# Optimization experiments

Hardware: AMD Instinct MI355X
Metric: run time of the kernel (lower is better)

The kernel has to match this reference:

```python
import jax, jax.numpy as jnp
import numpy as np

D_MODEL = 1024
NUM_HEADS = 16
SEQ = 2048
BATCH = 4
THETA = 10000.0
D_K = D_MODEL // NUM_HEADS


def setup_inputs() -> dict:
    key = jax.random.key(0)
    k1, k2, k3, k4, k5 = jax.random.split(key, 5)
    std = np.sqrt(2.0 / (D_MODEL + D_MODEL))
    x = jax.random.normal(k1, (BATCH, SEQ, D_MODEL), dtype=jnp.float32)
    wq = jax.random.normal(k2, (D_MODEL, D_MODEL), dtype=jnp.float32) * std
    wk = jax.random.normal(k3, (D_MODEL, D_MODEL), dtype=jnp.float32) * std
    wv = jax.random.normal(k4, (D_MODEL, D_MODEL), dtype=jnp.float32) * std
    wo = jax.random.normal(k5, (D_MODEL, D_MODEL), dtype=jnp.float32) * std
    token_positions = jnp.arange(SEQ, dtype=jnp.int32)
    return {"x": x, "wq": wq, "wk": wk, "wv": wv, "wo": wo,
            "token_positions": token_positions}


def _apply_rope(t, cos, sin):
    # t: (b, h, s, d_k); cos/sin: (s, d_k/2) -> broadcast over (b, h)
    pairs = t.reshape(*t.shape[:-1], D_K // 2, 2)
    x0, x1 = pairs[..., 0], pairs[..., 1]
    r0 = x0 * cos - x1 * sin
    r1 = x0 * sin + x1 * cos
    return jnp.stack((r0, r1), axis=-1).reshape(t.shape)


def reference(x, wq, wk, wv, wo, token_positions):
    b, s, d = x.shape
    h, dk = NUM_HEADS, D_K

    def split_heads(y):  # (b, s, d) -> (b, h, s, d_k)
        return y.reshape(b, s, h, dk).transpose(0, 2, 1, 3)

    q = split_heads(x @ wq.T)
    k = split_heads(x @ wk.T)
    v = split_heads(x @ wv.T)

    # RoPE tables: angles_j = theta^{-(2j)/d_k}, j = 0..d_k/2-1
    inv_freq = 1.0 / (THETA ** (jnp.arange(0, dk, 2, dtype=jnp.float32) / dk))
    ang = token_positions.astype(jnp.float32)[:, None] * inv_freq[None, :]  # (s, d_k/2)
    cos, sin = jnp.cos(ang), jnp.sin(ang)
    q = _apply_rope(q, cos, sin)
    k = _apply_rope(k, cos, sin)

    scores = jnp.einsum('bhqd,bhkd->bhqk', q, k) / jnp.sqrt(jnp.float32(dk))
    causal = jnp.tril(jnp.ones((s, s), dtype=bool))
    scores = jnp.where(causal, scores, -jnp.inf)
    attn = jax.nn.softmax(scores, axis=-1)
    out = jnp.einsum('bhqk,bhkd->bhqd', attn, v)  # (b, h, s, d_k)
    out = out.transpose(0, 2, 1, 3).reshape(b, s, d)
    return out @ wo.T
```

## Files before the change

### kernel.cpp

```cpp
#include <hip/hip_runtime.h>
#include <stdint.h>

#define B_   4
#define S_   2048
#define H_   16
#define DK_  64
#define DM_  1024
#define M_   (B_ * S_)

typedef __attribute__((ext_vector_type(4)))  float f32x4;
typedef __attribute__((ext_vector_type(16))) float f32x16;
typedef __attribute__((ext_vector_type(8)))  short s16x8;

__device__ __forceinline__ uint16_t f2bf(float f) {
    union { float f; uint32_t u; } v; v.f = f;
    uint32_t u = v.u;
    uint32_t r = (u + 0x7FFFu + ((u >> 16) & 1u)) >> 16;
    return (uint16_t)r;
}
__device__ __forceinline__ float bf2f(uint16_t h) {
    union { uint32_t u; float f; } v; v.u = ((uint32_t)h) << 16;
    return v.f;
}
__device__ __forceinline__ uint32_t cvt_pk_bf16(float lo, float hi) {
    uint32_t r;
    asm("v_cvt_pk_bf16_f32 %0, %1, %2" : "=v"(r) : "v"(lo), "v"(hi));
    return r;
}

__device__ __forceinline__ void gload_lds16(const uint16_t* g, uint16_t* l) {
    __builtin_amdgcn_global_load_lds(
        (const __attribute__((address_space(1))) void*)g,
        (__attribute__((address_space(3))) void*)l, 16, 0, 0);
}

__global__ __launch_bounds__(256) void cvt_bf16(const float* __restrict__ in,
                                                uint16_t* __restrict__ out, int n) {
    int i = (blockIdx.x * 256 + threadIdx.x) * 4;
    if (i >= n) return;
    float4 v = *reinterpret_cast<const float4*>(in + i);
    ushort4 o;
    o.x = f2bf(v.x); o.y = f2bf(v.y); o.z = f2bf(v.z); o.w = f2bf(v.w);
    *reinterpret_cast<ushort4*>(out + i) = o;
}

template <int MODE>
__global__ __launch_bounds__(256) void gemm_bt(const uint16_t* __restrict__ A,
                                               const uint16_t* __restrict__ Bm,
                                               void* __restrict__ Cout,
                                               int M, int N, int K) {
    __shared__ uint16_t Al[128 * 32];
    __shared__ uint16_t Bl[128 * 32];
    const int lane = threadIdx.x & 63;
    const int w    = threadIdx.x >> 6;
    const int wr   = w >> 1, wc = w & 1;
    const int m0   = blockIdx.x * 128;
    const int n0   = blockIdx.y * 128;
    const int lr   = lane & 15;
    const int lg   = lane >> 4;

    const int srow = w * 32 + (lane >> 2);
    const int scol = (lane & 3) * 8;
    const uint16_t* Ag = A  + (size_t)(m0 + srow) * K + scol;
    const uint16_t* Bg = Bm + (size_t)(n0 + srow) * K + scol;
    uint16_t* Ald = Al + (size_t)(w * 32) * 32;
    uint16_t* Bld = Bl + (size_t)(w * 32) * 32;

    f32x4 acc[4][4] = {};
    for (int k0 = 0; k0 < K; k0 += 32) {
        gload_lds16(Ag + k0,                  Ald);
        gload_lds16(Ag + 16 * (size_t)K + k0, Ald + 16 * 32);
        gload_lds16(Bg + k0,                  Bld);
        gload_lds16(Bg + 16 * (size_t)K + k0, Bld + 16 * 32);
        __syncthreads();
        s16x8 af[4], bfr[4];
#pragma unroll
        for (int i = 0; i < 4; ++i)
            af[i] = *reinterpret_cast<const s16x8*>(&Al[(wr * 64 + i * 16 + lr) * 32 + lg * 8]);
#pragma unroll
        for (int j = 0; j < 4; ++j)
            bfr[j] = *reinterpret_cast<const s16x8*>(&Bl[(wc * 64 + j * 16 + lr) * 32 + lg * 8]);
#pragma unroll
        for (int i = 0; i < 4; ++i)
#pragma unroll
            for (int j = 0; j < 4; ++j)
                acc[i][j] = __builtin_amdgcn_mfma_f32_16x16x32_bf16(af[i], bfr[j],
                                                                    acc[i][j], 0, 0, 0);
        __syncthreads();
    }

#pragma unroll
    for (int i = 0; i < 4; ++i)
#pragma unroll
        for (int j = 0; j < 4; ++j)
#pragma unroll
            for (int r = 0; r < 4; ++r) {
                int row = wr * 64 + m0 + i * 16 + lg * 4 + r;
                int col = wc * 64 + n0 + j * 16 + lr;
                float v = acc[i][j][r];
                if constexpr (MODE == 0) {
                    ((float*)Cout)[(size_t)row * N + col] = v;
                } else if constexpr (MODE == 1) {
                    int b = row >> 11, s = row & (S_ - 1);
                    int h = col >> 6,  dk = col & 63;
                    ((uint16_t*)Cout)[(((size_t)(b * H_ + h)) * S_ + s) * DK_ + dk] = f2bf(v);
                } else {
                    int h = row >> 6,  dk = row & 63;
                    int b = col >> 11, s = col & (S_ - 1);
                    ((uint16_t*)Cout)[(((size_t)(b * H_ + h)) * DK_ + dk) * S_ + s] = f2bf(v);
                }
            }
}

__global__ __launch_bounds__(256) void gemm_qk(const uint16_t* __restrict__ A,
                                               const uint16_t* __restrict__ wq,
                                               const uint16_t* __restrict__ wk,
                                               uint16_t* __restrict__ qout,
                                               uint16_t* __restrict__ kout) {
    __shared__ uint16_t Al[128 * 32];
    __shared__ uint16_t Bl[128 * 32];
    const int K = DM_;
    const int lane = threadIdx.x & 63;
    const int w    = threadIdx.x >> 6;
    const int wr   = w >> 1, wc = w & 1;
    const int m0   = blockIdx.x * 128;
    const int sel  = blockIdx.y >> 3;
    const int n0   = (blockIdx.y & 7) * 128;
    const uint16_t* Bw = sel ? wk : wq;
    uint16_t* dst      = sel ? kout : qout;
    const int lr   = lane & 15;
    const int lg   = lane >> 4;

    const int srow = w * 32 + (lane >> 2);
    const int scol = (lane & 3) * 8;
    const uint16_t* Ag = A  + (size_t)(m0 + srow) * K + scol;
    const uint16_t* Bg = Bw + (size_t)(n0 + srow) * K + scol;
    uint16_t* Ald = Al + (size_t)(w * 32) * 32;
    uint16_t* Bld = Bl + (size_t)(w * 32) * 32;

    f32x4 acc[4][4] = {};
    for (int k0 = 0; k0 < K; k0 += 32) {
        gload_lds16(Ag + k0,                  Ald);
        gload_lds16(Ag + 16 * (size_t)K + k0, Ald + 16 * 32);
        gload_lds16(Bg + k0,                  Bld);
        gload_lds16(Bg + 16 * (size_t)K + k0, Bld + 16 * 32);
        __syncthreads();
        s16x8 af[4], bfr[4];
#pragma unroll
        for (int i = 0; i < 4; ++i)
            af[i] = *reinterpret_cast<const s16x8*>(&Al[(wr * 64 + i * 16 + lr) * 32 + lg * 8]);
#pragma unroll
        for (int j = 0; j < 4; ++j)
            bfr[j] = *reinterpret_cast<const s16x8*>(&Bl[(wc * 64 + j * 16 + lr) * 32 + lg * 8]);
#pragma unroll
        for (int i = 0; i < 4; ++i)
#pragma unroll
            for (int j = 0; j < 4; ++j)
                acc[i][j] = __builtin_amdgcn_mfma_f32_16x16x32_bf16(af[i], bfr[j],
                                                                    acc[i][j], 0, 0, 0);
        __syncthreads();
    }

#pragma unroll
    for (int i = 0; i < 4; ++i)
#pragma unroll
        for (int j = 0; j < 4; ++j)
#pragma unroll
            for (int r = 0; r < 4; ++r) {
                int row = wr * 64 + m0 + i * 16 + lg * 4 + r;
                int col = wc * 64 + n0 + j * 16 + lr;
                int b = row >> 11, s = row & (S_ - 1);
                int h = col >> 6,  dk = col & 63;
                dst[(((size_t)(b * H_ + h)) * S_ + s) * DK_ + dk] = f2bf(acc[i][j][r]);
            }
}

__global__ __launch_bounds__(256) void rope_kernel(uint16_t* __restrict__ a,
                                                   const int* __restrict__ pos,
                                                   int npairs) {
    int t = blockIdx.x * 256 + threadIdx.x;
    if (t >= npairs) return;
    int j = t & 31;
    int s = (t >> 5) & (S_ - 1);
    float p   = (float)pos[s];
    float inv = exp2f(-(float)j * (13.287712379549449f / 32.0f));
    float ang = p * inv;
    float sn, c;
    sincosf(ang, &sn, &c);
    uint32_t pr = *reinterpret_cast<uint32_t*>(a + (size_t)2 * t);
    float x0 = bf2f((uint16_t)(pr & 0xFFFF));
    float x1 = bf2f((uint16_t)(pr >> 16));
    float r0 = x0 * c - x1 * sn;
    float r1 = x0 * sn + x1 * c;
    uint32_t ot = (uint32_t)f2bf(r0) | ((uint32_t)f2bf(r1) << 16);
    *reinterpret_cast<uint32_t*>(a + (size_t)2 * t) = ot;
}

__global__ __launch_bounds__(256, 2) void flash_attn(const uint16_t* __restrict__ qg,
                                                     const uint16_t* __restrict__ kg,
                                                     const uint16_t* __restrict__ vtg,
                                                     uint16_t* __restrict__ attn) {
    __shared__ __align__(16) uint16_t Kl[2][4096];
    __shared__ __align__(16) uint16_t Vl[2][4096];
    __shared__ __align__(16) uint16_t obuf[4][2048];
    const int lane = threadIdx.x & 63;
    const int w    = threadIdx.x >> 6;
    const int ql   = lane & 31;
    const int hi   = lane >> 5;
    const int id   = blockIdx.x;
    const int bh   = (id & 7) * 8 + ((id >> 3) & 7);
    const int s    = 15 - (id >> 6);
    const int b    = bh >> 4, hh = bh & 15;

    const uint16_t* kb_ = kg  + (size_t)bh * S_ * DK_;
    const uint16_t* vb_ = vtg + (size_t)bh * DK_ * S_;
    const float SC = 0.18033688011112042f;

    char* obb = (char*)&obuf[w][0];
    const int swz = (ql & 7) << 4;

    const int q0 = s * 128 + w * 32;
    const int rowg  = q0 + ql;
    const int ntmax = 2 * s + 2;

    const int srow = lane >> 3;
    const int scol = ((lane & 7) ^ srow) << 3;

    const uint16_t* qp = qg + ((size_t)bh * S_ + q0 + ql) * DK_ + hi * 8;
    s16x8 qf[4];
#pragma unroll
    for (int kk = 0; kk < 4; ++kk)
        qf[kk] = *reinterpret_cast<const s16x8*>(qp + kk * 16);

    f32x16 o0 = {}, o1 = {};
    float l_l = 0.f;

#pragma unroll
    for (int i = 0; i < 2; ++i) {
        gload_lds16(kb_ + (size_t)(w * 16 + i * 8 + srow) * DK_ + scol, &Kl[0][w * 1024 + i * 512]);
        gload_lds16(vb_ + (size_t)(w * 16 + i * 8 + srow) * S_  + scol, &Vl[0][w * 1024 + i * 512]);
    }

    for (int t = 0; t < ntmax; ++t) {
        const int kt  = t * 64;
        const int cur = t & 1;
        __syncthreads();
        if (t + 1 < ntmax) {
            const int kt2 = kt + 64, nb = cur ^ 1;
#pragma unroll
            for (int i = 0; i < 2; ++i) {
                gload_lds16(kb_ + (size_t)(kt2 + w * 16 + i * 8 + srow) * DK_ + scol,
                            &Kl[nb][w * 1024 + i * 512]);
                gload_lds16(vb_ + (size_t)(w * 16 + i * 8 + srow) * S_ + kt2 + scol,
                            &Vl[nb][w * 1024 + i * 512]);
            }
        }
        if (kt > q0 + 31) continue;

        s16x8 kf[8];
#pragma unroll
        for (int kb2 = 0; kb2 < 2; ++kb2)
#pragma unroll
            for (int kk = 0; kk < 4; ++kk)
                kf[kb2 * 4 + kk] = *reinterpret_cast<const s16x8*>(
                    &Kl[cur][(kb2 * 32 + ql) * 64 + (((kk * 32 + hi * 16) ^ swz) >> 1)]);

        f32x16 sc0 = {}, sc1 = {};
        __builtin_amdgcn_s_setprio(1);
#pragma unroll
        for (int kk = 0; kk < 4; ++kk)
            sc0 = __builtin_amdgcn_mfma_f32_32x32x16_bf16(kf[kk], qf[kk], sc0, 0, 0, 0);
#pragma unroll
        for (int kk = 0; kk < 4; ++kk)
            sc1 = __builtin_amdgcn_mfma_f32_32x32x16_bf16(kf[4 + kk], qf[kk], sc1, 0, 0, 0);
        __builtin_amdgcn_s_setprio(0);

        if (kt + 63 > q0) {
            const int keybase = kt + 4 * hi;
#pragma unroll
            for (int r = 0; r < 16; ++r) {
                const int cr = (r & 3) + 8 * (r >> 2);
                if (keybase + cr > rowg)      sc0[r] = -3e38f;
                if (keybase + cr + 32 > rowg) sc1[r] = -3e38f;
            }
        }

#pragma unroll
        for (int r = 0; r < 16; ++r) {
            float p0 = exp2f(sc0[r] * SC);
            float p1 = exp2f(sc1[r] * SC);
            sc0[r] = p0; sc1[r] = p1;
            l_l += p0 + p1;
        }

        s16x8 pf[4];
        {
            union PW { uint32_t u[4]; s16x8 v; };
#pragma unroll
            for (int half = 0; half < 2; ++half) {
                const f32x16& e = half ? sc1 : sc0;
#pragma unroll
                for (int sl = 0; sl < 2; ++sl) {
                    const int rb = sl * 8;
                    uint32_t a0 = cvt_pk_bf16(e[rb + 0], e[rb + 1]);
                    uint32_t b0 = cvt_pk_bf16(e[rb + 4], e[rb + 5]);
                    uint32_t a1 = cvt_pk_bf16(e[rb + 2], e[rb + 3]);
                    uint32_t b1 = cvt_pk_bf16(e[rb + 6], e[rb + 7]);
                    asm("v_permlane32_swap_b32 %0, %1" : "+v"(a0), "+v"(b0));
                    asm("v_permlane32_swap_b32 %0, %1" : "+v"(a1), "+v"(b1));
                    PW pw; pw.u[0] = a0; pw.u[1] = a1; pw.u[2] = b0; pw.u[3] = b1;
                    pf[half * 2 + sl] = pw.v;
                }
            }
        }

        s16x8 vf[8];
#pragma unroll
        for (int db = 0; db < 2; ++db)
#pragma unroll
            for (int ks = 0; ks < 4; ++ks)
                vf[db * 4 + ks] = *reinterpret_cast<const s16x8*>(
                    &Vl[cur][(db * 32 + ql) * 64 + (((ks * 32 + hi * 16) ^ swz) >> 1)]);

        __builtin_amdgcn_s_setprio(1);
#pragma unroll
        for (int ks = 0; ks < 4; ++ks) {
            o0 = __builtin_amdgcn_mfma_f32_32x32x16_bf16(vf[ks],     pf[ks], o0, 0, 0, 0);
            o1 = __builtin_amdgcn_mfma_f32_32x32x16_bf16(vf[4 + ks], pf[ks], o1, 0, 0, 0);
        }
        __builtin_amdgcn_s_setprio(0);
    }

    l_l += __shfl_xor(l_l, 32);
    float rinv = 1.0f / l_l;

#pragma unroll
    for (int db = 0; db < 2; ++db) {
        const f32x16& o = db ? o1 : o0;
#pragma unroll
        for (int rq = 0; rq < 4; ++rq) {
            uint2 val;
            val.x = cvt_pk_bf16(o[4 * rq + 0] * rinv, o[4 * rq + 1] * rinv);
            val.y = cvt_pk_bf16(o[4 * rq + 2] * rinv, o[4 * rq + 3] * rinv);
            int colb = (db * 32 + 8 * rq + 4 * hi) * 2;
            *reinterpret_cast<uint2*>(obb + ql * 128 + (colb ^ swz)) = val;
        }
    }
    uint16_t* orow = attn + ((size_t)b * S_ + q0 + ql) * DM_ + hh * 64 + hi * 32;
#pragma unroll
    for (int i = 0; i < 4; ++i) {
        int colb = hi * 64 + i * 16;
        s16x8 vrow = *reinterpret_cast<const s16x8*>(obb + ql * 128 + (colb ^ swz));
        *reinterpret_cast<s16x8*>(orow + i * 8) = vrow;
    }
}

extern "C" void kernel_launch(void* const* d_in, const int* in_sizes, int n_in,
                              void* d_out, int out_size, void* d_ws, size_t ws_size,
                              hipStream_t stream) {
    (void)in_sizes; (void)n_in; (void)out_size;
    const float* x   = (const float*)d_in[0];
    const float* wq  = (const float*)d_in[1];
    const float* wk  = (const float*)d_in[2];
    const float* wv  = (const float*)d_in[3];
    const float* wo  = (const float*)d_in[4];
    const int* tpos  = (const int*)d_in[5];
    float* out = (float*)d_out;

    const size_t NX = (size_t)M_ * DM_;
    const size_t NW = (size_t)DM_ * DM_;
    const size_t need = (NX + 4 * NW + 4 * NX) * sizeof(uint16_t);
    if (ws_size < need) return;

    uint16_t* ws  = (uint16_t*)d_ws;
    uint16_t* xb  = ws;
    uint16_t* wqb = xb + NX;
    uint16_t* wkb = wqb + NW;
    uint16_t* wvb = wkb + NW;
    uint16_t* wob = wvb + NW;
    uint16_t* qb  = wob + NW;
    uint16_t* kb  = qb + NX;
    uint16_t* vtb = kb + NX;
    uint16_t* ab  = vtb + NX;

    cvt_bf16<<<(int)(NX / 1024), 256, 0, stream>>>(x, xb, (int)NX);
    cvt_bf16<<<(int)(NW / 1024), 256, 0, stream>>>(wq, wqb, (int)NW);
    cvt_bf16<<<(int)(NW / 1024), 256, 0, stream>>>(wk, wkb, (int)NW);
    cvt_bf16<<<(int)(NW / 1024), 256, 0, stream>>>(wv, wvb, (int)NW);
    cvt_bf16<<<(int)(NW / 1024), 256, 0, stream>>>(wo, wob, (int)NW);

    dim3 blk(256);
    gemm_qk<<<dim3(M_ / 128, 16), blk, 0, stream>>>(xb, wqb, wkb, qb, kb);
    gemm_bt<3><<<dim3(DM_ / 128, M_ / 128), blk, 0, stream>>>(wvb, xb, vtb, DM_, M_, DM_);

    int npairs = 2 * B_ * H_ * S_ * (DK_ / 2);
    rope_kernel<<<npairs / 256, 256, 0, stream>>>(qb, tpos, npairs);

    flash_attn<<<dim3(1024), 256, 0, stream>>>(qb, kb, vtb, ab);

    gemm_bt<0><<<dim3(M_ / 128, DM_ / 128), blk, 0, stream>>>(ab, wob, out, M_, DM_, DM_);
}
```

Baseline: 211.4 us.

## Fuse QKV projections and weight casts, fold softmax scale into Q

Merges the four weight-conversion launches into one kernel and the Q/K and V projection GEMMs into a single launch covering all three outputs. The softmax scale (including log2e) is folded into Q at the projection epilogue, which removes a multiply per score in flash attention. The per-wave output staging buffer in attention now reuses the K shared-memory region behind an added barrier, lowering LDS use and possibly raising occupancy. Risks are extra bf16 rounding from pre-scaling Q before RoPE and the new synchronisation cost.

```diff
diff --git a/kernel.cpp b/kernel.cpp
--- a/kernel.cpp
+++ b/kernel.cpp
@@ -11,6 +11,8 @@
 typedef __attribute__((ext_vector_type(4)))  float f32x4;
 typedef __attribute__((ext_vector_type(16))) float f32x16;
 typedef __attribute__((ext_vector_type(8)))  short s16x8;
+
+#define SCQ 0.18033688011112042f
 
 __device__ __forceinline__ uint16_t f2bf(float f) {
     union { float f; uint32_t u; } v; v.f = f;
@@ -44,11 +46,106 @@
     *reinterpret_cast<ushort4*>(out + i) = o;
 }
 
-template <int MODE>
-__global__ __launch_bounds__(256) void gemm_bt(const uint16_t* __restrict__ A,
-                                               const uint16_t* __restrict__ Bm,
-                                               void* __restrict__ Cout,
-                                               int M, int N, int K) {
+__global__ __launch_bounds__(256) void cvt_w4(const float* __restrict__ w0,
+                                              const float* __restrict__ w1,
+                                              const float* __restrict__ w2,
+                                              const float* __restrict__ w3,
+                                              uint16_t* __restrict__ o0,
+                                              uint16_t* __restrict__ o1,
+                                              uint16_t* __restrict__ o2,
+                                              uint16_t* __restrict__ o3) {
+    const size_t NW = (size_t)DM_ * DM_;
+    size_t i = ((size_t)blockIdx.x * 256 + threadIdx.x) * 4;
+    int sel = (int)(i >> 20);
+    size_t off = i & (NW - 1);
+    const float* in = sel == 0 ? w0 : sel == 1 ? w1 : sel == 2 ? w2 : w3;
+    uint16_t* out   = sel == 0 ? o0 : sel == 1 ? o1 : sel == 2 ? o2 : o3;
+    float4 v = *reinterpret_cast<const float4*>(in + off);
+    ushort4 o;
+    o.x = f2bf(v.x); o.y = f2bf(v.y); o.z = f2bf(v.z); o.w = f2bf(v.w);
+    *reinterpret_cast<ushort4*>(out + off) = o;
+}
+
+__global__ __launch_bounds__(256) void gemm_qkv(const uint16_t* __restrict__ xb,
+                                                const uint16_t* __restrict__ wq,
+                                                const uint16_t* __restrict__ wk,
+                                                const uint16_t* __restrict__ wv,
+                                                uint16_t* __restrict__ qout,
+                                                uint16_t* __restrict__ kout,
+                                                uint16_t* __restrict__ vout) {
+    __shared__ uint16_t Al[128 * 32];
+    __shared__ uint16_t Bl[128 * 32];
+    const int K = DM_;
+    const int lane = threadIdx.x & 63;
+    const int w    = threadIdx.x >> 6;
+    const int wr   = w >> 1, wc = w & 1;
+    const int sel  = blockIdx.x >> 3;
+    const int np   = blockIdx.x & 7;
+    const int y    = blockIdx.y;
+    const int lr   = lane & 15;
+    const int lg   = lane >> 4;
+
+    const uint16_t* Aptr; const uint16_t* Bptr;
+    int m0, n0;
+    if (sel == 2) { Aptr = wv; Bptr = xb; m0 = np * 128; n0 = y * 128; }
+    else          { Aptr = xb; Bptr = sel ? wk : wq; m0 = y * 128; n0 = np * 128; }
+
+    const int srow = w * 32 + (lane >> 2);
+    const int scol = (lane & 3) * 8;
+    const uint16_t* Ag = Aptr + (size_t)(m0 + srow) * K + scol;
+    const uint16_t* Bg = Bptr + (size_t)(n0 + srow) * K + scol;
+    uint16_t* Ald = Al + (size_t)(w * 32) * 32;
+    uint16_t* Bld = Bl + (size_t)(w * 32) * 32;
+
+    f32x4 acc[4][4] = {};
+    for (int k0 = 0; k0 < K; k0 += 32) {
+        gload_lds16(Ag + k0,                  Ald);
+        gload_lds16(Ag + 16 * (size_t)K + k0, Ald + 16 * 32);
+        gload_lds16(Bg + k0,                  Bld);
+        gload_lds16(Bg + 16 * (size_t)K + k0, Bld + 16 * 32);
+        __syncthreads();
+        s16x8 af[4], bfr[4];
+#pragma unroll
+        for (int i = 0; i < 4; ++i)
+            af[i] = *reinterpret_cast<const s16x8*>(&Al[(wr * 64 + i * 16 + lr) * 32 + lg * 8]);
+#pragma unroll
+        for (int j = 0; j < 4; ++j)
+            bfr[j] = *reinterpret_cast<const s16x8*>(&Bl[(wc * 64 + j * 16 + lr) * 32 + lg * 8]);
+#pragma unroll
+        for (int i = 0; i < 4; ++i)
+#pragma unroll
+            for (int j = 0; j < 4; ++j)
+                acc[i][j] = __builtin_amdgcn_mfma_f32_16x16x32_bf16(af[i], bfr[j],
+                                                                    acc[i][j], 0, 0, 0);
+        __syncthreads();
+    }
+
+#pragma unroll
+    for (int i = 0; i < 4; ++i)
+#pragma unroll
+        for (int j = 0; j < 4; ++j)
+#pragma unroll
+            for (int r = 0; r < 4; ++r) {
+                int row = m0 + wr * 64 + i * 16 + lg * 4 + r;
+                int col = n0 + wc * 64 + j * 16 + lr;
+                float v = acc[i][j][r];
+                if (sel == 2) {
+                    int h = row >> 6,  dk = row & 63;
+                    int b = col >> 11, s = col & (S_ - 1);
+                    vout[(((size_t)(b * H_ + h)) * DK_ + dk) * S_ + s] = f2bf(v);
+                } else {
+                    int b = row >> 11, s = row & (S_ - 1);
+                    int h = col >> 6,  dk = col & 63;
+                    uint16_t bv = f2bf(sel ? v : v * SCQ);
+                    (sel ? kout : qout)[(((size_t)(b * H_ + h)) * S_ + s) * DK_ + dk] = bv;
+                }
+            }
+}
+
+__global__ __launch_bounds__(256) void gemm_out(const uint16_t* __restrict__ A,
+                                                const uint16_t* __restrict__ Bm,
+                                                float* __restrict__ Cout,
+                                                int M, int N, int K) {
     __shared__ uint16_t Al[128 * 32];
     __shared__ uint16_t Bl[128 * 32];
     const int lane = threadIdx.x & 63;
@@ -95,83 +192,9 @@
         for (int j = 0; j < 4; ++j)
 #pragma unroll
             for (int r = 0; r < 4; ++r) {
-                int row = wr * 64 + m0 + i * 16 + lg * 4 + r;
-                int col = wc * 64 + n0 + j * 16 + lr;
-                float v = acc[i][j][r];
-                if constexpr (MODE == 0) {
-                    ((float*)Cout)[(size_t)row * N + col] = v;
-                } else if constexpr (MODE == 1) {
-                    int b = row >> 11, s = row & (S_ - 1);
-                    int h = col >> 6,  dk = col & 63;
-                    ((uint16_t*)Cout)[(((size_t)(b * H_ + h)) * S_ + s) * DK_ + dk] = f2bf(v);
-                } else {
-                    int h = row >> 6,  dk = row & 63;
-                    int b = col >> 11, s = col & (S_ - 1);
-                    ((uint16_t*)Cout)[(((size_t)(b * H_ + h)) * DK_ + dk) * S_ + s] = f2bf(v);
-                }
-            }
-}
-
-__global__ __launch_bounds__(256) void gemm_qk(const uint16_t* __restrict__ A,
-                                               const uint16_t* __restrict__ wq,
-                                               const uint16_t* __restrict__ wk,
-                                               uint16_t* __restrict__ qout,
-                                               uint16_t* __restrict__ kout) {
-    __shared__ uint16_t Al[128 * 32];
-    __shared__ uint16_t Bl[128 * 32];
-    const int K = DM_;
-    const int lane = threadIdx.x & 63;
-    const int w    = threadIdx.x >> 6;
-    const int wr   = w >> 1, wc = w & 1;
-    const int m0   = blockIdx.x * 128;
-    const int sel  = blockIdx.y >> 3;
-    const int n0   = (blockIdx.y & 7) * 128;
-    const uint16_t* Bw = sel ? wk : wq;
-    uint16_t* dst      = sel ? kout : qout;
-    const int lr   = lane & 15;
-    const int lg   = lane >> 4;
-
-    const int srow = w * 32 + (lane >> 2);
-    const int scol = (lane & 3) * 8;
-    const uint16_t* Ag = A  + (size_t)(m0 + srow) * K + scol;
-    const uint16_t* Bg = Bw + (size_t)(n0 + srow) * K + scol;
-    uint16_t* Ald = Al + (size_t)(w * 32) * 32;
-    uint16_t* Bld = Bl + (size_t)(w * 32) * 32;
-
-    f32x4 acc[4][4] = {};
-    for (int k0 = 0; k0 < K; k0 += 32) {
-        gload_lds16(Ag + k0,                  Ald);
-        gload_lds16(Ag + 16 * (size_t)K + k0, Ald + 16 * 32);
-        gload_lds16(Bg + k0,                  Bld);
-        gload_lds16(Bg + 16 * (size_t)K + k0, Bld + 16 * 32);
-        __syncthreads();
-        s16x8 af[4], bfr[4];
-#pragma unroll
-        for (int i = 0; i < 4; ++i)
-            af[i] = *reinterpret_cast<const s16x8*>(&Al[(wr * 64 + i * 16 + lr) * 32 + lg * 8]);
-#pragma unroll
-        for (int j = 0; j < 4; ++j)
-            bfr[j] = *reinterpret_cast<const s16x8*>(&Bl[(wc * 64 + j * 16 + lr) * 32 + lg * 8]);
-#pragma unroll
-        for (int i = 0; i < 4; ++i)
-#pragma unroll
-            for (int j = 0; j < 4; ++j)
-                acc[i][j] = __builtin_amdgcn_mfma_f32_16x16x32_bf16(af[i], bfr[j],
-                                                                    acc[i][j], 0, 0, 0);
-        __syncthreads();
-    }
-
-#pragma unroll
-    for (int i = 0; i < 4; ++i)
-#pragma unroll
-        for (int j = 0; j < 4; ++j)
-#pragma unroll
-            for (int r = 0; r < 4; ++r) {
-                int row = wr * 64 + m0 + i * 16 + lg * 4 + r;
-                int col = wc * 64 + n0 + j * 16 + lr;
-                int b = row >> 11, s = row & (S_ - 1);
-                int h = col >> 6,  dk = col & 63;
-                dst[(((size_t)(b * H_ + h)) * S_ + s) * DK_ + dk] = f2bf(acc[i][j][r]);
+                int row = m0 + wr * 64 + i * 16 + lg * 4 + r;
+                int col = n0 + wc * 64 + j * 16 + lr;
+                Cout[(size_t)row * N + col] = acc[i][j][r];
             }
 }
 
@@ -202,7 +225,6 @@
                                                      uint16_t* __restrict__ attn) {
     __shared__ __align__(16) uint16_t Kl[2][4096];
     __shared__ __align__(16) uint16_t Vl[2][4096];
-    __shared__ __align__(16) uint16_t obuf[4][2048];
     const int lane = threadIdx.x & 63;
     const int w    = threadIdx.x >> 6;
     const int ql   = lane & 31;
@@ -214,9 +236,8 @@
 
     const uint16_t* kb_ = kg  + (size_t)bh * S_ * DK_;
     const uint16_t* vb_ = vtg + (size_t)bh * DK_ * S_;
-    const float SC = 0.18033688011112042f;
-
-    char* obb = (char*)&obuf[w][0];
+
+    char* obb = (char*)&Kl[0][0] + w * 4096;
     const int swz = (ql & 7) << 4;
 
     const int q0 = s * 128 + w * 32;
@@ -287,8 +308,8 @@
 
 #pragma unroll
         for (int r = 0; r < 16; ++r) {
-            float p0 = exp2f(sc0[r] * SC);
-            float p1 = exp2f(sc1[r] * SC);
+            float p0 = exp2f(sc0[r]);
+            float p1 = exp2f(sc1[r]);
             sc0[r] = p0; sc1[r] = p1;
             l_l += p0 + p1;
         }
@@ -331,6 +352,8 @@
         __builtin_amdgcn_s_setprio(0);
     }
 
+    __syncthreads();
+
     l_l += __shfl_xor(l_l, 32);
     float rinv = 1.0f / l_l;
 
@@ -384,19 +407,14 @@
     uint16_t* ab  = vtb + NX;
 
     cvt_bf16<<<(int)(NX / 1024), 256, 0, stream>>>(x, xb, (int)NX);
-    cvt_bf16<<<(int)(NW / 1024), 256, 0, stream>>>(wq, wqb, (int)NW);
-    cvt_bf16<<<(int)(NW / 1024), 256, 0, stream>>>(wk, wkb, (int)NW);
-    cvt_bf16<<<(int)(NW / 1024), 256, 0, stream>>>(wv, wvb, (int)NW);
-    cvt_bf16<<<(int)(NW / 1024), 256, 0, stream>>>(wo, wob, (int)NW);
-
-    dim3 blk(256);
-    gemm_qk<<<dim3(M_ / 128, 16), blk, 0, stream>>>(xb, wqb, wkb, qb, kb);
-    gemm_bt<3><<<dim3(DM_ / 128, M_ / 128), blk, 0, stream>>>(wvb, xb, vtb, DM_, M_, DM_);
+    cvt_w4<<<(int)(4 * NW / 1024), 256, 0, stream>>>(wq, wk, wv, wo, wqb, wkb, wvb, wob);
+
+    gemm_qkv<<<dim3(24, M_ / 128), 256, 0, stream>>>(xb, wqb, wkb, wvb, qb, kb, vtb);
 
     int npairs = 2 * B_ * H_ * S_ * (DK_ / 2);
     rope_kernel<<<npairs / 256, 256, 0, stream>>>(qb, tpos, npairs);
 
     flash_attn<<<dim3(1024), 256, 0, stream>>>(qb, kb, vtb, ab);
 
-    gemm_bt<0><<<dim3(M_ / 128, DM_ / 128), blk, 0, stream>>>(ab, wob, out, M_, DM_, DM_);
-}
+    gemm_out<<<dim3(M_ / 128, DM_ / 128), 256, 0, stream>>>(ab, wob, out, M_, DM_, DM_);
+}
```

Result: no change. 211.9 us (+0.2%).
